# Optimization experiments

Hardware: AMD Instinct MI355X
Metric: run time of the kernel (lower is better)

## Reference

```python
import jax, jax.numpy as jnp
import numpy as np

N_NODES = 50000
EMBED_DIM = 512
N_EDGES = 800000
NEG_SLOPE = 0.01  # nn.LeakyReLU default


def setup_inputs() -> dict:
    key = jax.random.key(0)
    k1, k2, k3 = jax.random.split(key, 3)
    X = jax.random.normal(k1, (N_NODES, EMBED_DIM), dtype=jnp.float32)
    # Glorot-ish scale for the GCNConv weight
    W = jax.random.normal(k2, (EMBED_DIM, EMBED_DIM), dtype=jnp.float32) / np.sqrt(EMBED_DIM)
    b = jnp.zeros((EMBED_DIM,), dtype=jnp.float32)
    edge_index = jax.random.randint(k3, (2, N_EDGES), 0, N_NODES, dtype=jnp.int32)
    return {"X": X, "W": W, "b": b, "edge_index": edge_index}


def reference(X, W, b, edge_index):
    N = X.shape[0]
    # GCNConv: add self-loops, symmetric normalization deg^-1/2 A deg^-1/2
    loop = jnp.arange(N, dtype=edge_index.dtype)
    src = jnp.concatenate([edge_index[0], loop])  # [E+N]
    dst = jnp.concatenate([edge_index[1], loop])  # [E+N]
    deg = jax.ops.segment_sum(jnp.ones_like(dst, dtype=X.dtype), dst, num_segments=N)
    dinv = jnp.where(deg > 0, jax.lax.rsqrt(deg), 0.0)  # deg^{-1/2}, inf->0
    norm = dinv[src] * dinv[dst]                         # [E+N]
    H = X @ W                                            # [N, D] dense GEMM
    msgs = H[src] * norm[:, None]                        # [E+N, D] gathered messages
    out = jax.ops.segment_sum(msgs, dst, num_segments=N) + b
    # LeakyReLU activation; Dropout is identity in eval mode
    return jnp.where(out >= 0, out, NEG_SLOPE * out)
```

## Files before the change

kernel.cpp:

```cpp
#include <hip/hip_runtime.h>
#include <cstdint>
#include <cstddef>

#define DFEAT 512
#define BM 128
#define BN 128
#define BK 32

typedef __attribute__((ext_vector_type(8))) short bf16x8;
typedef __attribute__((ext_vector_type(4))) float f32x4;

#define GLOBAL_AS __attribute__((address_space(1)))
#define LDS_AS __attribute__((address_space(3)))

__device__ __forceinline__ unsigned short f2bf(float f) {
  unsigned u = __float_as_uint(f);
  u = u + 0x7fffu + ((u >> 16) & 1u);
  return (unsigned short)(u >> 16);
}

__device__ __forceinline__ float bf2f_lo(unsigned u) { return __uint_as_float(u << 16); }
__device__ __forceinline__ float bf2f_hi(unsigned u) { return __uint_as_float(u & 0xffff0000u); }

__device__ __forceinline__ void gl_lds16(const void* g, void* l) {
  __builtin_amdgcn_global_load_lds((const GLOBAL_AS unsigned int*)g,
                                   (LDS_AS unsigned int*)l, 16, 0, 0);
}

__global__ void k_count(const int* __restrict__ dst, int* __restrict__ deg8,
                        int E, int N) {
  const int i = blockIdx.x * 256 + threadIdx.x;
  if (i < E) {
    const int d = __builtin_nontemporal_load(dst + i);
    atomicAdd(&deg8[(size_t)(blockIdx.x & 7) * N + d], 1);
  }
}

__global__ __launch_bounds__(1024) void k_scan(const int* __restrict__ deg8,
                                               int* __restrict__ deg,
                                               int* __restrict__ rowStart,
                                               int* __restrict__ fillPos, int N) {
  const int t = threadIdx.x;
  const int base = blockIdx.x * 1024;
  __shared__ int sm[1024];
  int pre = 0;
  for (int i = t; i < base; i += 1024) {
    int s = 0;
#pragma unroll
    for (int x = 0; x < 8; ++x) s += deg8[(size_t)x * N + i];
    pre += s;
  }
  sm[t] = pre;
  __syncthreads();
  for (int d = 512; d > 0; d >>= 1) {
    if (t < d) sm[t] += sm[t + d];
    __syncthreads();
  }
  const int blockBase = sm[0];
  __syncthreads();
  const int idx = base + t;
  int v = 0;
  if (idx < N) {
#pragma unroll
    for (int x = 0; x < 8; ++x) v += deg8[(size_t)x * N + idx];
    deg[idx] = v;
  }
  sm[t] = v;
  __syncthreads();
  for (int d = 1; d < 1024; d <<= 1) {
    const int o = (t >= d) ? sm[t - d] : 0;
    __syncthreads();
    sm[t] += o;
    __syncthreads();
  }
  if (idx < N) {
    const int ex = blockBase + sm[t] - v;
    rowStart[idx] = ex;
    fillPos[idx] = ex;
    if (idx == N - 1) rowStart[N] = ex + v;
  }
}

__global__ void k_fillcast(const int* __restrict__ src, const int* __restrict__ dst,
                           int* __restrict__ fillPos, int2* __restrict__ cw,
                           const int* __restrict__ deg, int E,
                           const float* __restrict__ W, unsigned short* __restrict__ Wt,
                           const float* __restrict__ X, unsigned short* __restrict__ Xb,
                           int total8) {
  const int fb = (E + 255) >> 8;
  int b = blockIdx.x;
  if (b < fb) {
    const int i = b * 256 + threadIdx.x;
    if (i < E) {
      const int d = dst[i], s = src[i];
      const int pos = atomicAdd(&fillPos[d], 1);
      int2 q; q.x = s; q.y = __float_as_int(rsqrtf((float)(deg[s] + 1)));
      cw[pos] = q;
    }
    return;
  }
  b -= fb;
  if (b < 1024) {
    const int i = b * 256 + threadIdx.x;
    const int k = i >> 9, n = i & 511;
    Wt[(size_t)n * DFEAT + k] = f2bf(W[i]);
    return;
  }
  b -= 1024;
  const int i = b * 256 + threadIdx.x;
  if (i >= total8) return;
  const f32x4 a = __builtin_nontemporal_load(reinterpret_cast<const f32x4*>(X + (size_t)i * 8));
  const f32x4 c = __builtin_nontemporal_load(reinterpret_cast<const f32x4*>(X + (size_t)i * 8 + 4));
  uint4 o;
  o.x = (unsigned)f2bf(a[0]) | ((unsigned)f2bf(a[1]) << 16);
  o.y = (unsigned)f2bf(a[2]) | ((unsigned)f2bf(a[3]) << 16);
  o.z = (unsigned)f2bf(c[0]) | ((unsigned)f2bf(c[1]) << 16);
  o.w = (unsigned)f2bf(c[2]) | ((unsigned)f2bf(c[3]) << 16);
  *reinterpret_cast<uint4*>(Xb + (size_t)i * 8) = o;
}

template <bool TAIL>
__device__ __forceinline__ void agg8(const unsigned short* __restrict__ Xb,
                                     const int2* __restrict__ cw,
                                     int p, int e, int lane, float* acc) {
  unsigned long long q[8];
#pragma unroll
  for (int i = 0; i < 8; ++i) {
    int pi = p + i;
    if (TAIL) pi = (pi < e) ? pi : (e - 1);
    q[i] = __builtin_nontemporal_load(reinterpret_cast<const unsigned long long*>(cw + pi));
  }
  uint4 v[8];
#pragma unroll
  for (int i = 0; i < 8; ++i)
    v[i] = *reinterpret_cast<const uint4*>(Xb + (size_t)(unsigned)q[i] * DFEAT + lane * 8);
#pragma unroll
  for (int i = 0; i < 8; ++i) {
    float w = __uint_as_float((unsigned)(q[i] >> 32));
    if (TAIL) w = (p + i < e) ? w : 0.0f;
    acc[0] = fmaf(w, bf2f_lo(v[i].x), acc[0]); acc[1] = fmaf(w, bf2f_hi(v[i].x), acc[1]);
    acc[2] = fmaf(w, bf2f_lo(v[i].y), acc[2]); acc[3] = fmaf(w, bf2f_hi(v[i].y), acc[3]);
    acc[4] = fmaf(w, bf2f_lo(v[i].z), acc[4]); acc[5] = fmaf(w, bf2f_hi(v[i].z), acc[5]);
    acc[6] = fmaf(w, bf2f_lo(v[i].w), acc[6]); acc[7] = fmaf(w, bf2f_hi(v[i].w), acc[7]);
  }
}

__global__ __launch_bounds__(256) void k_aggregate(const unsigned short* __restrict__ Xb,
                                                   const int2* __restrict__ cw,
                                                   const int* __restrict__ rowStart,
                                                   unsigned short* __restrict__ Y, int N) {
  const int row = blockIdx.x * 4 + (threadIdx.x >> 6);
  const int lane = threadIdx.x & 63;
  float acc[8] = {0.f, 0.f, 0.f, 0.f, 0.f, 0.f, 0.f, 0.f};
  if (row < N) {
    const int s = rowStart[row], e = rowStart[row + 1];
    const float sc = rsqrtf((float)(e - s + 1));
    const uint4 v0 = *reinterpret_cast<const uint4*>(Xb + (size_t)row * DFEAT + lane * 8);
    acc[0] = sc * bf2f_lo(v0.x); acc[1] = sc * bf2f_hi(v0.x);
    acc[2] = sc * bf2f_lo(v0.y); acc[3] = sc * bf2f_hi(v0.y);
    acc[4] = sc * bf2f_lo(v0.z); acc[5] = sc * bf2f_hi(v0.z);
    acc[6] = sc * bf2f_lo(v0.w); acc[7] = sc * bf2f_hi(v0.w);
    int p = s;
    for (; p + 8 <= e; p += 8) agg8<false>(Xb, cw, p, e, lane, acc);
    if (p < e) agg8<true>(Xb, cw, p, e, lane, acc);
#pragma unroll
    for (int j = 0; j < 8; ++j) acc[j] *= sc;
  }
  uint4 o;
  o.x = (unsigned)f2bf(acc[0]) | ((unsigned)f2bf(acc[1]) << 16);
  o.y = (unsigned)f2bf(acc[2]) | ((unsigned)f2bf(acc[3]) << 16);
  o.z = (unsigned)f2bf(acc[4]) | ((unsigned)f2bf(acc[5]) << 16);
  o.w = (unsigned)f2bf(acc[6]) | ((unsigned)f2bf(acc[7]) << 16);
  *reinterpret_cast<uint4*>(Y + (size_t)row * DFEAT + lane * 8) = o;
}

__global__ __launch_bounds__(256) void k_gemm(const unsigned short* __restrict__ Y,
                                              const unsigned short* __restrict__ Wt,
                                              const float* __restrict__ bias,
                                              float* __restrict__ out, int M) {
  __shared__ unsigned short As[BM * BK];
  __shared__ unsigned short Bs[BN * BK];
  const int tid = threadIdx.x;
  const int lane = tid & 63;
  const int wave = tid >> 6;
  const int l16 = lane & 15;
  const int quad = lane >> 4;
  const int wm = (wave >> 1) * 64;
  const int wn = (wave & 1) * 64;

  const int nwg = gridDim.x;
  const int q8 = nwg >> 3, r8 = nwg & 7;
  const int xcd = blockIdx.x & 7, loc = blockIdx.x >> 3;
  const int wg = (xcd < r8 ? xcd * (q8 + 1) : r8 * (q8 + 1) + (xcd - r8) * q8) + loc;
  const int m0 = (wg >> 2) * BM;
  const int n0 = (wg & 3) * BN;

  f32x4 acc[4][4];
#pragma unroll
  for (int mi = 0; mi < 4; ++mi)
#pragma unroll
    for (int ni = 0; ni < 4; ++ni) { f32x4 z = {0.f, 0.f, 0.f, 0.f}; acc[mi][ni] = z; }

  const int ci0 = wave * 64 + lane;
  const int ci1 = 256 + ci0;
  const int ra0 = ci0 >> 2, ka0 = (((ci0 & 3) - (ra0 >> 1)) & 3) * 8;
  const int ra1 = ci1 >> 2, ka1 = (((ci1 & 3) - (ra1 >> 1)) & 3) * 8;

  const unsigned short* Ag0 = Y + (size_t)(m0 + ra0) * DFEAT + ka0;
  const unsigned short* Ag1 = Y + (size_t)(m0 + ra1) * DFEAT + ka1;
  const unsigned short* Bg0 = Wt + (size_t)(n0 + ra0) * DFEAT + ka0;
  const unsigned short* Bg1 = Wt + (size_t)(n0 + ra1) * DFEAT + ka1;
  unsigned short* La0 = As + ci0 * 8;
  unsigned short* La1 = As + ci1 * 8;
  unsigned short* Lb0 = Bs + ci0 * 8;
  unsigned short* Lb1 = Bs + ci1 * 8;

  const int rotA = (quad + ((wm + l16) >> 1)) & 3;
  const int rotB = (quad + ((wn + l16) >> 1)) & 3;
  const unsigned short* AsRd = As + (wm + l16) * BK + rotA * 8;
  const unsigned short* BsRd = Bs + (wn + l16) * BK + rotB * 8;

  for (int kk = 0; kk < DFEAT; kk += BK) {
    gl_lds16(Ag0 + kk, La0);
    gl_lds16(Ag1 + kk, La1);
    gl_lds16(Bg0 + kk, Lb0);
    gl_lds16(Bg1 + kk, Lb1);
    __syncthreads();
    bf16x8 av[4], bv[4];
#pragma unroll
    for (int mi = 0; mi < 4; ++mi)
      av[mi] = *reinterpret_cast<const bf16x8*>(AsRd + mi * 16 * BK);
#pragma unroll
    for (int ni = 0; ni < 4; ++ni)
      bv[ni] = *reinterpret_cast<const bf16x8*>(BsRd + ni * 16 * BK);
#pragma unroll
    for (int mi = 0; mi < 4; ++mi)
#pragma unroll
      for (int ni = 0; ni < 4; ++ni)
        acc[mi][ni] = __builtin_amdgcn_mfma_f32_16x16x32_bf16(av[mi], bv[ni], acc[mi][ni], 0, 0, 0);
    __syncthreads();
  }

  float bvals[4];
#pragma unroll
  for (int ni = 0; ni < 4; ++ni) bvals[ni] = bias[n0 + wn + 16 * ni + l16];

#pragma unroll
  for (int mi = 0; mi < 4; ++mi) {
#pragma unroll
    for (int r = 0; r < 4; ++r) {
      int row = m0 + wm + 16 * mi + quad * 4 + r;
      if (row < M) {
#pragma unroll
        for (int ni = 0; ni < 4; ++ni) {
          float v = acc[mi][ni][r] + bvals[ni];
          v = (v >= 0.f) ? v : 0.01f * v;
          out[(size_t)row * DFEAT + n0 + wn + 16 * ni + l16] = v;
        }
      }
    }
  }
}

extern "C" void kernel_launch(void* const* d_in, const int* in_sizes, int n_in,
                              void* d_out, int out_size, void* d_ws, size_t ws_size,
                              hipStream_t stream) {
  const float* X = (const float*)d_in[0];
  const float* W = (const float*)d_in[1];
  const float* b = (const float*)d_in[2];
  const int* ei  = (const int*)d_in[3];
  const int D = DFEAT;
  const int N = in_sizes[0] / D;
  const int E = in_sizes[3] / 2;
  const int* src = ei;
  const int* dst = ei + E;
  float* out = (float*)d_out;

  uintptr_t p = (uintptr_t)d_ws;
  auto carve = [&](size_t bytes) -> void* {
    uintptr_t r = p;
    p += (bytes + 255) & ~(size_t)255;
    return (void*)r;
  };
  int*   deg8     = (int*)carve(sizeof(int) * (size_t)N * 8);
  int*   deg      = (int*)carve(sizeof(int) * (size_t)N);
  int*   rowStart = (int*)carve(sizeof(int) * (size_t)(N + 1));
  int*   fillPos  = (int*)carve(sizeof(int) * (size_t)N);
  int2*  cw       = (int2*)carve(sizeof(int2) * (size_t)E);
  unsigned short* Wt = (unsigned short*)carve(sizeof(unsigned short) * (size_t)D * D);
  const int Mtiles = (N + BM - 1) / BM;
  const int Mpad = Mtiles * BM;
  unsigned short* Y  = (unsigned short*)carve(sizeof(unsigned short) * (size_t)Mpad * D);

  unsigned short* Xb = (unsigned short*)d_out;

  const int total8 = N * D / 8;
  const int fb = (E + 255) / 256;
  const int xb = (total8 + 255) / 256;

  hipMemsetAsync(deg8, 0, sizeof(int) * (size_t)N * 8, stream);
  hipLaunchKernelGGL(k_count,    dim3((E + 255) / 256), dim3(256), 0, stream, dst, deg8, E, N);
  hipLaunchKernelGGL(k_scan,     dim3((N + 1023) / 1024), dim3(1024), 0, stream,
                     deg8, deg, rowStart, fillPos, N);
  hipLaunchKernelGGL(k_fillcast, dim3(fb + 1024 + xb), dim3(256), 0, stream,
                     src, dst, fillPos, cw, deg, E, W, Wt, X, Xb, total8);
  hipLaunchKernelGGL(k_aggregate, dim3(Mpad / 4), dim3(256), 0, stream,
                     Xb, cw, rowStart, Y, N);
  hipLaunchKernelGGL(k_gemm,     dim3(Mtiles * 4), dim3(256), 0, stream, Y, Wt, b, out, N);
}
```

Measured before the change: 435.0 us.

## Move X cast into degree-count kernel and interleave block roles

```diff
diff --git a/kernel.cpp b/kernel.cpp
--- a/kernel.cpp
+++ b/kernel.cpp
@@ -27,13 +27,30 @@
                                    (LDS_AS unsigned int*)l, 16, 0, 0);
 }
 
-__global__ void k_count(const int* __restrict__ dst, int* __restrict__ deg8,
-                        int E, int N) {
-  const int i = blockIdx.x * 256 + threadIdx.x;
-  if (i < E) {
-    const int d = __builtin_nontemporal_load(dst + i);
-    atomicAdd(&deg8[(size_t)(blockIdx.x & 7) * N + d], 1);
-  }
+__global__ void k_countcast(const int* __restrict__ dst, int* __restrict__ deg8,
+                            int E, int N,
+                            const float* __restrict__ X, unsigned short* __restrict__ Xb,
+                            int total8) {
+  const int b = blockIdx.x;
+  const int m = b % 5;
+  if (m == 4) {
+    const int i = (b / 5) * 256 + threadIdx.x;
+    if (i < E) {
+      const int d = __builtin_nontemporal_load(dst + i);
+      atomicAdd(&deg8[(size_t)(b & 7) * N + d], 1);
+    }
+    return;
+  }
+  const int i = ((b / 5) * 4 + m) * 256 + threadIdx.x;
+  if (i >= total8) return;
+  const f32x4 a = __builtin_nontemporal_load(reinterpret_cast<const f32x4*>(X + (size_t)i * 8));
+  const f32x4 c = __builtin_nontemporal_load(reinterpret_cast<const f32x4*>(X + (size_t)i * 8 + 4));
+  uint4 o;
+  o.x = (unsigned)f2bf(a[0]) | ((unsigned)f2bf(a[1]) << 16);
+  o.y = (unsigned)f2bf(a[2]) | ((unsigned)f2bf(a[3]) << 16);
+  o.z = (unsigned)f2bf(c[0]) | ((unsigned)f2bf(c[1]) << 16);
+  o.w = (unsigned)f2bf(c[2]) | ((unsigned)f2bf(c[3]) << 16);
+  *reinterpret_cast<uint4*>(Xb + (size_t)i * 8) = o;
 }
 
 __global__ __launch_bounds__(1024) void k_scan(const int* __restrict__ deg8,
@@ -81,42 +98,27 @@
   }
 }
 
-__global__ void k_fillcast(const int* __restrict__ src, const int* __restrict__ dst,
-                           int* __restrict__ fillPos, int2* __restrict__ cw,
-                           const int* __restrict__ deg, int E,
-                           const float* __restrict__ W, unsigned short* __restrict__ Wt,
-                           const float* __restrict__ X, unsigned short* __restrict__ Xb,
-                           int total8) {
-  const int fb = (E + 255) >> 8;
-  int b = blockIdx.x;
-  if (b < fb) {
-    const int i = b * 256 + threadIdx.x;
-    if (i < E) {
-      const int d = dst[i], s = src[i];
-      const int pos = atomicAdd(&fillPos[d], 1);
-      int2 q; q.x = s; q.y = __float_as_int(rsqrtf((float)(deg[s] + 1)));
-      cw[pos] = q;
+__global__ void k_fillwt(const int* __restrict__ src, const int* __restrict__ dst,
+                         int* __restrict__ fillPos, int2* __restrict__ cw,
+                         const int* __restrict__ deg, int E,
+                         const float* __restrict__ W, unsigned short* __restrict__ Wt) {
+  const int b = blockIdx.x;
+  const int m = b & 3;
+  if (m == 3) {
+    const int i = (b >> 2) * 256 + threadIdx.x;
+    if (i < DFEAT * DFEAT) {
+      const int k = i >> 9, n = i & 511;
+      Wt[(size_t)n * DFEAT + k] = f2bf(W[i]);
     }
     return;
   }
-  b -= fb;
-  if (b < 1024) {
-    const int i = b * 256 + threadIdx.x;
-    const int k = i >> 9, n = i & 511;
-    Wt[(size_t)n * DFEAT + k] = f2bf(W[i]);
-    return;
-  }
-  b -= 1024;
-  const int i = b * 256 + threadIdx.x;
-  if (i >= total8) return;
-  const f32x4 a = __builtin_nontemporal_load(reinterpret_cast<const f32x4*>(X + (size_t)i * 8));
-  const f32x4 c = __builtin_nontemporal_load(reinterpret_cast<const f32x4*>(X + (size_t)i * 8 + 4));
-  uint4 o;
-  o.x = (unsigned)f2bf(a[0]) | ((unsigned)f2bf(a[1]) << 16);
-  o.y = (unsigned)f2bf(a[2]) | ((unsigned)f2bf(a[3]) << 16);
-  o.z = (unsigned)f2bf(c[0]) | ((unsigned)f2bf(c[1]) << 16);
-  o.w = (unsigned)f2bf(c[2]) | ((unsigned)f2bf(c[3]) << 16);
-  *reinterpret_cast<uint4*>(Xb + (size_t)i * 8) = o;
+  const int i = ((b >> 2) * 3 + m) * 256 + threadIdx.x;
+  if (i < E) {
+    const int d = dst[i], s = src[i];
+    const int pos = atomicAdd(&fillPos[d], 1);
+    int2 q; q.x = s; q.y = __float_as_int(rsqrtf((float)(deg[s] + 1)));
+    cw[pos] = q;
+  }
 }
 
 template <bool TAIL>
@@ -297,14 +299,21 @@
   const int total8 = N * D / 8;
   const int fb = (E + 255) / 256;
   const int xb = (total8 + 255) / 256;
+  const int wb = (D * D + 255) / 256;
+
+  const int xq = (xb + 3) / 4;
+  const int nA = 5 * (fb > xq ? fb : xq);
+  const int fq = (fb + 2) / 3;
+  const int nB = 4 * (fq > wb ? fq : wb);
 
   hipMemsetAsync(deg8, 0, sizeof(int) * (size_t)N * 8, stream);
-  hipLaunchKernelGGL(k_count,    dim3((E + 255) / 256), dim3(256), 0, stream, dst, deg8, E, N);
-  hipLaunchKernelGGL(k_scan,     dim3((N + 1023) / 1024), dim3(1024), 0, stream,
+  hipLaunchKernelGGL(k_countcast, dim3(nA), dim3(256), 0, stream,
+                     dst, deg8, E, N, X, Xb, total8);
+  hipLaunchKernelGGL(k_scan,      dim3((N + 1023) / 1024), dim3(1024), 0, stream,
                      deg8, deg, rowStart, fillPos, N);
-  hipLaunchKernelGGL(k_fillcast, dim3(fb + 1024 + xb), dim3(256), 0, stream,
-                     src, dst, fillPos, cw, deg, E, W, Wt, X, Xb, total8);
+  hipLaunchKernelGGL(k_fillwt,    dim3(nB), dim3(256), 0, stream,
+                     src, dst, fillPos, cw, deg, E, W, Wt);
   hipLaunchKernelGGL(k_aggregate, dim3(Mpad / 4), dim3(256), 0, stream,
                      Xb, cw, rowStart, Y, N);
-  hipLaunchKernelGGL(k_gemm,     dim3(Mtiles * 4), dim3(256), 0, stream, Y, Wt, b, out, N);
-}
+  hipLaunchKernelGGL(k_gemm,      dim3(Mtiles * 4), dim3(256), 0, stream, Y, Wt, b, out, N);
+}
```

New measurement: 413.5 us. 1.05x faster.
